# Kernel optimization log

Hardware: AMD Instinct MI355X
Metric: run time of the kernel (lower is better)

Reference implementation:

```python
import jax, jax.numpy as jnp
import numpy as np

D_MODEL = 2048
EPS = 1e-05


def setup_inputs() -> dict:
    key = jax.random.key(0)
    x = jax.random.normal(key, (4, 4096, D_MODEL), dtype=jnp.float32)
    gain = jnp.ones((D_MODEL,), dtype=jnp.float32)
    return {"x": x, "gain": gain}


def reference(x, gain):
    # rms over last dim: sqrt(mean(x^2) + eps); note torch code divides sum by d_model
    rms = jnp.sqrt(jnp.mean(jnp.square(x), axis=-1, keepdims=True) + EPS)
    return (x / rms) * gain
```

## Files before the change

kernel.cpp:

```cpp
#include <hip/hip_runtime.h>

#define D_MODEL 2048
#define EPS 1e-5f

__global__ __launch_bounds__(256) void rmsnorm_kernel(
    const float* __restrict__ x,
    const float* __restrict__ gain,
    float* __restrict__ out)
{
    const size_t row = blockIdx.x;
    const float* __restrict__ xr = x + row * (size_t)D_MODEL;
    float* __restrict__ orow = out + row * (size_t)D_MODEL;
    const int t = threadIdx.x;

    const float4 a = *reinterpret_cast<const float4*>(xr + t * 4);
    const float4 b = *reinterpret_cast<const float4*>(xr + 1024 + t * 4);

    float ss = a.x * a.x + a.y * a.y + a.z * a.z + a.w * a.w
             + b.x * b.x + b.y * b.y + b.z * b.z + b.w * b.w;

    #pragma unroll
    for (int off = 32; off > 0; off >>= 1)
        ss += __shfl_xor(ss, off, 64);

    __shared__ float wave_sums[4];
    const int lane = t & 63;
    const int wave = t >> 6;
    if (lane == 0) wave_sums[wave] = ss;
    __syncthreads();
    const float total = wave_sums[0] + wave_sums[1] + wave_sums[2] + wave_sums[3];

    const float scale = rsqrtf(total * (1.0f / (float)D_MODEL) + EPS);

    const float4 g0 = *reinterpret_cast<const float4*>(gain + t * 4);
    const float4 g1 = *reinterpret_cast<const float4*>(gain + 1024 + t * 4);

    float4 o0, o1;
    o0.x = a.x * scale * g0.x;
    o0.y = a.y * scale * g0.y;
    o0.z = a.z * scale * g0.z;
    o0.w = a.w * scale * g0.w;
    o1.x = b.x * scale * g1.x;
    o1.y = b.y * scale * g1.y;
    o1.z = b.z * scale * g1.z;
    o1.w = b.w * scale * g1.w;

    *reinterpret_cast<float4*>(orow + t * 4) = o0;
    *reinterpret_cast<float4*>(orow + 1024 + t * 4) = o1;
}

extern "C" void kernel_launch(void* const* d_in, const int* in_sizes, int n_in,
                              void* d_out, int out_size, void* d_ws, size_t ws_size,
                              hipStream_t stream) {
    const float* x = (const float*)d_in[0];
    const float* gain = (const float*)d_in[1];
    float* out = (float*)d_out;

    const int rows = in_sizes[0] / D_MODEL;
    rmsnorm_kernel<<<rows, 256, 0, stream>>>(x, gain, out);
}
```

Before: 43.35 us.

## Map one wavefront per row and use nontemporal output stores

```diff
diff --git a/kernel.cpp b/kernel.cpp
--- a/kernel.cpp
+++ b/kernel.cpp
@@ -2,51 +2,47 @@
 
 #define D_MODEL 2048
 #define EPS 1e-5f
+
+typedef float f32x4 __attribute__((ext_vector_type(4)));
 
 __global__ __launch_bounds__(256) void rmsnorm_kernel(
     const float* __restrict__ x,
     const float* __restrict__ gain,
     float* __restrict__ out)
 {
-    const size_t row = blockIdx.x;
+    const int wave_in_block = threadIdx.x >> 6;
+    const int lane = threadIdx.x & 63;
+    const size_t row = (size_t)blockIdx.x * 4 + wave_in_block;
+
     const float* __restrict__ xr = x + row * (size_t)D_MODEL;
     float* __restrict__ orow = out + row * (size_t)D_MODEL;
-    const int t = threadIdx.x;
 
-    const float4 a = *reinterpret_cast<const float4*>(xr + t * 4);
-    const float4 b = *reinterpret_cast<const float4*>(xr + 1024 + t * 4);
+    f32x4 v[8];
+    #pragma unroll
+    for (int c = 0; c < 8; ++c)
+        v[c] = *reinterpret_cast<const f32x4*>(xr + c * 256 + lane * 4);
 
-    float ss = a.x * a.x + a.y * a.y + a.z * a.z + a.w * a.w
-             + b.x * b.x + b.y * b.y + b.z * b.z + b.w * b.w;
+    float ss = 0.0f;
+    #pragma unroll
+    for (int c = 0; c < 8; ++c)
+        ss += v[c].x * v[c].x + v[c].y * v[c].y + v[c].z * v[c].z + v[c].w * v[c].w;
 
     #pragma unroll
     for (int off = 32; off > 0; off >>= 1)
         ss += __shfl_xor(ss, off, 64);
 
-    __shared__ float wave_sums[4];
-    const int lane = t & 63;
-    const int wave = t >> 6;
-    if (lane == 0) wave_sums[wave] = ss;
-    __syncthreads();
-    const float total = wave_sums[0] + wave_sums[1] + wave_sums[2] + wave_sums[3];
+    const float scale = rsqrtf(ss * (1.0f / (float)D_MODEL) + EPS);
 
-    const float scale = rsqrtf(total * (1.0f / (float)D_MODEL) + EPS);
-
-    const float4 g0 = *reinterpret_cast<const float4*>(gain + t * 4);
-    const float4 g1 = *reinterpret_cast<const float4*>(gain + 1024 + t * 4);
-
-    float4 o0, o1;
-    o0.x = a.x * scale * g0.x;
-    o0.y = a.y * scale * g0.y;
-    o0.z = a.z * scale * g0.z;
-    o0.w = a.w * scale * g0.w;
-    o1.x = b.x * scale * g1.x;
-    o1.y = b.y * scale * g1.y;
-    o1.z = b.z * scale * g1.z;
-    o1.w = b.w * scale * g1.w;
-
-    *reinterpret_cast<float4*>(orow + t * 4) = o0;
-    *reinterpret_cast<float4*>(orow + 1024 + t * 4) = o1;
+    #pragma unroll
+    for (int c = 0; c < 8; ++c) {
+        const f32x4 g = *reinterpret_cast<const f32x4*>(gain + c * 256 + lane * 4);
+        f32x4 o;
+        o.x = v[c].x * scale * g.x;
+        o.y = v[c].y * scale * g.y;
+        o.z = v[c].z * scale * g.z;
+        o.w = v[c].w * scale * g.w;
+        __builtin_nontemporal_store(o, reinterpret_cast<f32x4*>(orow + c * 256 + lane * 4));
+    }
 }
 
 extern "C" void kernel_launch(void* const* d_in, const int* in_sizes, int n_in,
@@ -57,5 +53,5 @@
     float* out = (float*)d_out;
 
     const int rows = in_sizes[0] / D_MODEL;
-    rmsnorm_kernel<<<rows, 256, 0, stream>>>(x, gain, out);
+    rmsnorm_kernel<<<rows / 4, 256, 0, stream>>>(x, gain, out);
 }
```

New measurement: 43.72 us. Within noise of the previous version (+0.9%).
